# Performance work log

Hardware: AMD Instinct MI355X
Metric: run time of the kernel (lower is better)

The kernel has to match this reference:

```python
import jax, jax.numpy as jnp
import numpy as np

DIM = 768
HEADS = 12
HEAD_DIM = DIM // HEADS
HIDDEN = 4 * DIM
EPS = 1e-5
SCALE = HEAD_DIM ** -0.5


def _ln(x, g, b):
    mu = jnp.mean(x, axis=-1, keepdims=True)
    var = jnp.var(x, axis=-1, keepdims=True)
    return (x - mu) * jax.lax.rsqrt(var + EPS) * g + b


def setup_inputs() -> dict:
    key = jax.random.key(0)
    ks = jax.random.split(key, 10)
    s = lambda fan_in: 1.0 / np.sqrt(fan_in)
    return {
        "x": jax.random.normal(ks[0], (8, 4, 512, DIM), dtype=jnp.float32),
        "g1": jnp.ones((DIM,), jnp.float32),
        "b1": jnp.zeros((DIM,), jnp.float32),
        "Wqkv": jax.random.normal(ks[1], (DIM, 3 * DIM), jnp.float32) * s(DIM),
        "Wp": jax.random.normal(ks[2], (DIM, DIM), jnp.float32) * s(DIM),
        "bp": jnp.zeros((DIM,), jnp.float32),
        "g2": jnp.ones((DIM,), jnp.float32),
        "b2": jnp.zeros((DIM,), jnp.float32),
        "W1": jax.random.normal(ks[3], (DIM, HIDDEN), jnp.float32) * s(DIM),
        "bm1": jnp.zeros((HIDDEN,), jnp.float32),
        "W2": jax.random.normal(ks[4], (HIDDEN, DIM), jnp.float32) * s(HIDDEN),
        "bm2": jnp.zeros((DIM,), jnp.float32),
    }


def reference(x, g1, b1, Wqkv, Wp, bp, g2, b2, W1, bm1, W2, bm2):
    B, S, N, D = x.shape
    h = _ln(x, g1, b1)
    qkv = h @ Wqkv                                   # [B,S,N,3D]
    qkv = qkv.reshape(B, S, N, 3, HEADS, HEAD_DIM)
    q, k, v = (qkv[..., i, :, :] for i in range(3))  # [B,S,N,H,Dh]
    # scores over tokens N, per head
    attn = jnp.einsum("bsnhd,bsmhd->bshnm", q, k) * SCALE
    attn = jax.nn.softmax(attn, axis=-1)
    y = jnp.einsum("bshnm,bsmhd->bsnhd", attn, v).reshape(B, S, N, D)
    y = y @ Wp + bp
    x = x + y
    h2 = _ln(x, g2, b2)
    m = jax.nn.gelu(h2 @ W1 + bm1, approximate=False) @ W2 + bm2
    return x + m
```

## Files before the change

### kernel.cpp

```cpp
#include <hip/hip_runtime.h>
#include <hip/hip_bf16.h>
#include <cstdint>


typedef __bf16 bf16;
typedef bf16 bf16x8 __attribute__((ext_vector_type(8)));
typedef float f32x4 __attribute__((ext_vector_type(4)));
typedef uint32_t u32;

__device__ __forceinline__ f32x4 mfma16(bf16x8 a, bf16x8 b, f32x4 c){
  return __builtin_amdgcn_mfma_f32_16x16x32_bf16(a, b, c, 0, 0, 0);
}

__device__ __forceinline__ void gload16(const void* g, const void* l){
  __builtin_amdgcn_global_load_lds(
      (__attribute__((address_space(1))) u32*)(uintptr_t)g,
      (__attribute__((address_space(3))) u32*)(u32)(uintptr_t)l,
      16, 0, 0);
}

__global__ __launch_bounds__(256)
void transpose_cast(const float* __restrict__ W, bf16* __restrict__ Wt, int K, int N)
{
  __shared__ float t[64][65];
  int n0 = blockIdx.x * 64, k0 = blockIdx.y * 64;
  int tid = threadIdx.x;
  int c = tid & 63, r4 = tid >> 6;
#pragma unroll
  for (int i = 0; i < 16; ++i){
    int r = r4 * 16 + i;
    t[r][c] = W[(size_t)(k0 + r) * N + n0 + c];
  }
  __syncthreads();
#pragma unroll
  for (int i = 0; i < 16; ++i){
    int r = r4 * 16 + i;
    Wt[(size_t)(n0 + r) * K + k0 + c] = (bf16)t[c][r];
  }
}

__global__ __launch_bounds__(256)
void ln_kernel(const float* __restrict__ x, const float* __restrict__ g,
               const float* __restrict__ b, bf16* __restrict__ out)
{
  int row = blockIdx.x;
  int tid = threadIdx.x;
  const float* xr = x + (size_t)row * 768;
  float v0 = xr[tid], v1 = xr[tid + 256], v2 = xr[tid + 512];
  float s = v0 + v1 + v2;
  float ss = v0*v0 + v1*v1 + v2*v2;
#pragma unroll
  for (int m = 1; m < 64; m <<= 1){
    s  += __shfl_xor(s,  m, 64);
    ss += __shfl_xor(ss, m, 64);
  }
  __shared__ float red[8];
  int w = tid >> 6, l = tid & 63;
  if (l == 0){ red[w] = s; red[4 + w] = ss; }
  __syncthreads();
  s  = red[0] + red[1] + red[2] + red[3];
  ss = red[4] + red[5] + red[6] + red[7];
  float mu  = s * (1.0f / 768.0f);
  float var = ss * (1.0f / 768.0f) - mu * mu;
  float rs  = rsqrtf(var + 1e-5f);
  bf16* o = out + (size_t)row * 768;
  o[tid]       = (bf16)((v0 - mu) * rs * g[tid]       + b[tid]);
  o[tid + 256] = (bf16)((v1 - mu) * rs * g[tid + 256] + b[tid + 256]);
  o[tid + 512] = (bf16)((v2 - mu) * rs * g[tid + 512] + b[tid + 512]);
}

template<int EPI>
__global__ __launch_bounds__(256)
void gemm128(const bf16* __restrict__ A, const bf16* __restrict__ Bt,
             const float* __restrict__ bias, const float* __restrict__ res,
             void* __restrict__ Cout, int M, int N, int K)
{
  __shared__ bf16 Al[128 * 32];
  __shared__ bf16 Bl[128 * 32];
  int nbn = N >> 7;
  int nwg = gridDim.x;
  int cpx = nwg >> 3;
  int bid = (int)blockIdx.x;
  int sw  = (bid & 7) * cpx + (bid >> 3);
  int bm = sw / nbn, bn = sw % nbn;
  int tid = threadIdx.x;
  int w = tid >> 6, l = tid & 63;
  int wr = w >> 1, wc = w & 1;
  int lr = l & 15, lg = l >> 4;
  size_t rowA = (size_t)bm * 128, colB = (size_t)bn * 128;

  f32x4 acc[4][4];
#pragma unroll
  for (int m = 0; m < 4; ++m)
#pragma unroll
    for (int n = 0; n < 4; ++n) acc[m][n] = f32x4{0.f, 0.f, 0.f, 0.f};

  int rsub = l >> 2;
  int ksub = (l & 3) * 8;

  for (int kt = 0; kt < K; kt += 32){
    __syncthreads();
#pragma unroll
    for (int i = 0; i < 2; ++i){
      int sg = w * 2 + i;
      gload16(A  + (rowA + sg * 16 + rsub) * K + kt + ksub, &Al[sg * 512]);
      gload16(Bt + (colB + sg * 16 + rsub) * K + kt + ksub, &Bl[sg * 512]);
    }
    __syncthreads();
    bf16x8 af[4], bfr[4];
#pragma unroll
    for (int m = 0; m < 4; ++m)
      af[m]  = *(const bf16x8*)&Al[(wr * 64 + m * 16 + lr) * 32 + lg * 8];
#pragma unroll
    for (int n = 0; n < 4; ++n)
      bfr[n] = *(const bf16x8*)&Bl[(wc * 64 + n * 16 + lr) * 32 + lg * 8];
#pragma unroll
    for (int m = 0; m < 4; ++m)
#pragma unroll
      for (int n = 0; n < 4; ++n)
        acc[m][n] = mfma16(af[m], bfr[n], acc[m][n]);
  }

  size_t crow = rowA + wr * 64;
  size_t ccol = colB + wc * 64;
#pragma unroll
  for (int m = 0; m < 4; ++m){
#pragma unroll
    for (int n = 0; n < 4; ++n){
      size_t r0 = crow + m * 16 + lg * 4;
      size_t c  = ccol + n * 16 + lr;
#pragma unroll
      for (int i = 0; i < 4; ++i){
        size_t r = r0 + i;
        float v = acc[m][n][i];
        if (EPI == 0){
          ((bf16*)Cout)[r * (size_t)N + c] = (bf16)v;
        } else if (EPI == 1){
          v += bias[c];
          v = 0.5f * v * (1.0f + erff(v * 0.70710678118654752f));
          ((bf16*)Cout)[r * (size_t)N + c] = (bf16)v;
        } else {
          v += bias[c] + res[r * (size_t)N + c];
          ((float*)Cout)[r * (size_t)N + c] = v;
        }
      }
    }
  }
}

__global__ __launch_bounds__(256)
void attn_kernel(const bf16* __restrict__ qkv, bf16* __restrict__ y)
{
  int bid = blockIdx.x;
  int qt  = bid & 7;
  int bsh = bid >> 3;
  int h = bsh % 12;
  int R = bsh / 12;
  size_t rowbase = (size_t)R * 512;
  int tid = threadIdx.x, w = tid >> 6, l = tid & 63;
  int lr = l & 15, lg = l >> 4;

  __shared__ bf16 Kl[64 * 64];
  __shared__ bf16 Vt[64 * 64];
  __shared__ bf16 Pl[4][16 * 64];

  int q0 = qt * 64 + w * 16;
  bf16x8 qf[2];
#pragma unroll
  for (int ks = 0; ks < 2; ++ks)
    qf[ks] = *(const bf16x8*)&qkv[(rowbase + q0 + lr) * 2304 + h * 64 + ks * 32 + lg * 8];

  float mi[4], li[4];
  f32x4 oa[4];
#pragma unroll
  for (int i = 0; i < 4; ++i){ mi[i] = -1e30f; li[i] = 0.f; }
#pragma unroll
  for (int dt = 0; dt < 4; ++dt) oa[dt] = f32x4{0.f, 0.f, 0.f, 0.f};

  for (int c = 0; c < 8; ++c){
    __syncthreads();
    size_t tokbase = rowbase + c * 64;
#pragma unroll
    for (int it = 0; it < 2; ++it){
      int idx = it * 256 + tid;
      int t  = idx >> 3;
      int c8 = idx & 7;
      bf16x8 kv = *(const bf16x8*)&qkv[(tokbase + t) * 2304 + 768 + h * 64 + c8 * 8];
      *(bf16x8*)&Kl[t * 64 + ((c8 ^ (t & 7)) * 8)] = kv;
      bf16x8 vv = *(const bf16x8*)&qkv[(tokbase + t) * 2304 + 1536 + h * 64 + c8 * 8];
#pragma unroll
      for (int j = 0; j < 8; ++j){
        int d = c8 * 8 + j;
        Vt[d * 64 + (((t >> 3) ^ (d & 7)) * 8) + (t & 7)] = vv[j];
      }
    }
    __syncthreads();

    f32x4 s[4];
#pragma unroll
    for (int tt = 0; tt < 4; ++tt){
      f32x4 a = f32x4{0.f, 0.f, 0.f, 0.f};
#pragma unroll
      for (int ks = 0; ks < 2; ++ks){
        int row = tt * 16 + lr;
        int c8 = ks * 4 + lg;
        bf16x8 kf = *(const bf16x8*)&Kl[row * 64 + ((c8 ^ (row & 7)) * 8)];
        a = mfma16(qf[ks], kf, a);
      }
      s[tt] = a * 0.125f;
    }

    float pr[4][4];
#pragma unroll
    for (int i = 0; i < 4; ++i){
      float rm = fmaxf(fmaxf(s[0][i], s[1][i]), fmaxf(s[2][i], s[3][i]));
#pragma unroll
      for (int mm = 1; mm < 16; mm <<= 1) rm = fmaxf(rm, __shfl_xor(rm, mm, 64));
      float mn = fmaxf(mi[i], rm);
      float corr = __expf(mi[i] - mn);
      float rs = 0.f;
#pragma unroll
      for (int tt = 0; tt < 4; ++tt){
        float p = __expf(s[tt][i] - mn);
        pr[tt][i] = p;
        rs += p;
      }
#pragma unroll
      for (int mm = 1; mm < 16; mm <<= 1) rs += __shfl_xor(rs, mm, 64);
      li[i] = li[i] * corr + rs;
#pragma unroll
      for (int dt = 0; dt < 4; ++dt) oa[dt][i] *= corr;
      mi[i] = mn;
    }

#pragma unroll
    for (int i = 0; i < 4; ++i){
      int qr = lg * 4 + i;
#pragma unroll
      for (int tt = 0; tt < 4; ++tt){
        int tok = tt * 16 + lr;
        Pl[w][qr * 64 + (((tok >> 3) ^ (qr & 7)) * 8) + (tok & 7)] = (bf16)pr[tt][i];
      }
    }
    __syncthreads();

#pragma unroll
    for (int ks = 0; ks < 2; ++ks){
      bf16x8 pf = *(const bf16x8*)&Pl[w][lr * 64 + (((ks * 4 + lg) ^ (lr & 7)) * 8)];
#pragma unroll
      for (int dt = 0; dt < 4; ++dt){
        int row = dt * 16 + lr;
        int c8 = ks * 4 + lg;
        bf16x8 vf = *(const bf16x8*)&Vt[row * 64 + ((c8 ^ (row & 7)) * 8)];
        oa[dt] = mfma16(pf, vf, oa[dt]);
      }
    }
  }

#pragma unroll
  for (int i = 0; i < 4; ++i){
    float inv = 1.0f / li[i];
    size_t r = rowbase + q0 + lg * 4 + i;
#pragma unroll
    for (int dt = 0; dt < 4; ++dt)
      y[r * 768 + h * 64 + dt * 16 + lr] = (bf16)(oa[dt][i] * inv);
  }
}

extern "C" void kernel_launch(void* const* d_in, const int* in_sizes, int n_in,
                              void* d_out, int out_size, void* d_ws, size_t ws_size,
                              hipStream_t stream)
{
  (void)in_sizes; (void)n_in; (void)out_size; (void)ws_size;
  const float* x    = (const float*)d_in[0];
  const float* g1   = (const float*)d_in[1];
  const float* b1   = (const float*)d_in[2];
  const float* Wqkv = (const float*)d_in[3];
  const float* Wp   = (const float*)d_in[4];
  const float* bp   = (const float*)d_in[5];
  const float* g2   = (const float*)d_in[6];
  const float* b2   = (const float*)d_in[7];
  const float* W1   = (const float*)d_in[8];
  const float* bm1  = (const float*)d_in[9];
  const float* W2   = (const float*)d_in[10];
  const float* bm2  = (const float*)d_in[11];
  float* out = (float*)d_out;

  char* ws = (char*)d_ws;
  size_t off = 0;
  auto alloc = [&](size_t nbytes) -> void* {
    void* p = ws + off;
    off += (nbytes + 255) & ~(size_t)255;
    return p;
  };
  bf16* WqkvT = (bf16*)alloc((size_t)2304 * 768 * 2);
  bf16* WpT   = (bf16*)alloc((size_t)768 * 768 * 2);
  bf16* W1T   = (bf16*)alloc((size_t)3072 * 768 * 2);
  bf16* W2T   = (bf16*)alloc((size_t)768 * 3072 * 2);
  char* R1 = (char*)alloc((size_t)16384 * 768 * 2);
  char* R2 = (char*)alloc((size_t)16384 * 3072 * 2);
  bf16* h   = (bf16*)R1;
  bf16* yb  = (bf16*)R1;
  bf16* h2  = (bf16*)R1;
  bf16* qkv = (bf16*)R2;
  bf16* m1  = (bf16*)R2;
  float* x2 = out;

  transpose_cast<<<dim3(36, 12), dim3(256), 0, stream>>>(Wqkv, WqkvT, 768, 2304);
  transpose_cast<<<dim3(12, 12), dim3(256), 0, stream>>>(Wp,   WpT,   768, 768);
  transpose_cast<<<dim3(48, 12), dim3(256), 0, stream>>>(W1,   W1T,   768, 3072);
  transpose_cast<<<dim3(12, 48), dim3(256), 0, stream>>>(W2,   W2T,   3072, 768);

  ln_kernel<<<dim3(16384), dim3(256), 0, stream>>>(x, g1, b1, h);
  gemm128<0><<<dim3(2304), dim3(256), 0, stream>>>(h, WqkvT, nullptr, nullptr,
                                                   (void*)qkv, 16384, 2304, 768);
  attn_kernel<<<dim3(3072), dim3(256), 0, stream>>>(qkv, yb);
  gemm128<2><<<dim3(768), dim3(256), 0, stream>>>(yb, WpT, bp, x,
                                                  (void*)x2, 16384, 768, 768);
  ln_kernel<<<dim3(16384), dim3(256), 0, stream>>>(x2, g2, b2, h2);
  gemm128<1><<<dim3(3072), dim3(256), 0, stream>>>(h2, W1T, bm1, nullptr,
                                                   (void*)m1, 16384, 3072, 768);
  gemm128<2><<<dim3(768), dim3(256), 0, stream>>>(m1, W2T, bm2, x2,
                                                  (void*)out, 16384, 768, 3072);
}
```

Baseline: 700.6 us.

## Replace 128-tile GEMM with double-buffered 256x256 tile GEMM using swizzled LDS

```diff
diff --git a/kernel.cpp b/kernel.cpp
--- a/kernel.cpp
+++ b/kernel.cpp
@@ -70,69 +70,111 @@
 }
 
 template<int EPI>
-__global__ __launch_bounds__(256)
-void gemm128(const bf16* __restrict__ A, const bf16* __restrict__ Bt,
+__global__ __launch_bounds__(512, 2)
+void gemm256(const bf16* __restrict__ A, const bf16* __restrict__ Bt,
              const float* __restrict__ bias, const float* __restrict__ res,
              void* __restrict__ Cout, int M, int N, int K)
 {
-  __shared__ bf16 Al[128 * 32];
-  __shared__ bf16 Bl[128 * 32];
-  int nbn = N >> 7;
-  int nwg = gridDim.x;
-  int cpx = nwg >> 3;
-  int bid = (int)blockIdx.x;
-  int sw  = (bid & 7) * cpx + (bid >> 3);
-  int bm = sw / nbn, bn = sw % nbn;
-  int tid = threadIdx.x;
-  int w = tid >> 6, l = tid & 63;
-  int wr = w >> 1, wc = w & 1;
-  int lr = l & 15, lg = l >> 4;
-  size_t rowA = (size_t)bm * 128, colB = (size_t)bn * 128;
-
-  f32x4 acc[4][4];
-#pragma unroll
-  for (int m = 0; m < 4; ++m)
-#pragma unroll
-    for (int n = 0; n < 4; ++n) acc[m][n] = f32x4{0.f, 0.f, 0.f, 0.f};
-
-  int rsub = l >> 2;
-  int ksub = (l & 3) * 8;
-
-  for (int kt = 0; kt < K; kt += 32){
-    __syncthreads();
-#pragma unroll
-    for (int i = 0; i < 2; ++i){
-      int sg = w * 2 + i;
-      gload16(A  + (rowA + sg * 16 + rsub) * K + kt + ksub, &Al[sg * 512]);
-      gload16(Bt + (colB + sg * 16 + rsub) * K + kt + ksub, &Bl[sg * 512]);
-    }
-    __syncthreads();
-    bf16x8 af[4], bfr[4];
-#pragma unroll
-    for (int m = 0; m < 4; ++m)
-      af[m]  = *(const bf16x8*)&Al[(wr * 64 + m * 16 + lr) * 32 + lg * 8];
-#pragma unroll
-    for (int n = 0; n < 4; ++n)
-      bfr[n] = *(const bf16x8*)&Bl[(wc * 64 + n * 16 + lr) * 32 + lg * 8];
-#pragma unroll
-    for (int m = 0; m < 4; ++m)
-#pragma unroll
-      for (int n = 0; n < 4; ++n)
-        acc[m][n] = mfma16(af[m], bfr[n], acc[m][n]);
-  }
-
-  size_t crow = rowA + wr * 64;
-  size_t ccol = colB + wc * 64;
-#pragma unroll
-  for (int m = 0; m < 4; ++m){
-#pragma unroll
-    for (int n = 0; n < 4; ++n){
-      size_t r0 = crow + m * 16 + lg * 4;
-      size_t c  = ccol + n * 16 + lr;
+  extern __shared__ bf16 lds[];
+  const int tid = threadIdx.x;
+  const int w = tid >> 6, l = tid & 63;
+  const int lr = l & 15, lg = l >> 4;
+  const int wr = w >> 2, wc = w & 3;
+  const int nbm = M >> 8, nbn = N >> 8;
+  const int nwg = nbm * nbn;
+  const int cpx = nwg >> 3;
+  const int bid = (int)blockIdx.x;
+  const int sw  = (bid & 7) * cpx + (bid >> 3);
+  const int bm = sw % nbm, bn = sw / nbm;
+  const int rowA0 = bm << 8, colB0 = bn << 8;
+
+  f32x4 acc[8][4];
+#pragma unroll
+  for (int i = 0; i < 8; ++i)
+#pragma unroll
+    for (int j = 0; j < 4; ++j) acc[i][j] = f32x4{0.f, 0.f, 0.f, 0.f};
+
+  const int srow = l >> 3;
+  const int sg   = (l & 7) ^ srow;
+  auto stA = [&](int T, int q){
+    bf16* dst = lds + (size_t)(T & 1) * 32768 + q * 4096 + w * 512;
+    int row = q * 64 + w * 8 + srow;
+    gload16(A + (size_t)(rowA0 + row) * K + T * 64 + sg * 8, dst);
+  };
+  auto stB = [&](int T, int nh, int j){
+    int hh = j * 8 + w;
+    int row0 = (hh >> 2) * 64 + nh * 32 + (hh & 3) * 8;
+    bf16* dst = lds + (size_t)(T & 1) * 32768 + 16384 + row0 * 64;
+    int row = row0 + srow;
+    gload16(Bt + (size_t)(colB0 + row) * K + T * 64 + sg * 8, dst);
+  };
+
+  const int NT = K >> 6;
+
+  stA(0,0); stA(0,2); stB(0,0,0); stB(0,0,1);
+  stA(0,1); stA(0,3); stB(0,1,0); stB(0,1,1);
+  asm volatile("s_waitcnt vmcnt(4)" ::: "memory");
+  __builtin_amdgcn_s_barrier();
+
+#define PHASE(MH, NH, STAGE_STMT)                                              \
+  {                                                                            \
+    bf16x8 af[4][2], bfr[2][2];                                                \
+    _Pragma("unroll")                                                          \
+    for (int fr = 0; fr < 4; ++fr)                                             \
+      _Pragma("unroll")                                                        \
+      for (int kk = 0; kk < 2; ++kk){                                          \
+        int row = wr * 128 + (MH) * 64 + fr * 16 + lr;                         \
+        af[fr][kk] = *(const bf16x8*)&Abuf[row * 64 +                          \
+                       (((kk * 4 + lg) ^ (lr & 7)) << 3)];                     \
+      }                                                                        \
+    _Pragma("unroll")                                                          \
+    for (int fc = 0; fc < 2; ++fc)                                             \
+      _Pragma("unroll")                                                        \
+      for (int kk = 0; kk < 2; ++kk){                                          \
+        int row = wc * 64 + (NH) * 32 + fc * 16 + lr;                          \
+        bfr[fc][kk] = *(const bf16x8*)&Bbuf[row * 64 +                         \
+                       (((kk * 4 + lg) ^ (lr & 7)) << 3)];                     \
+      }                                                                        \
+    STAGE_STMT;                                                                \
+    if (more) asm volatile("s_waitcnt vmcnt(4)" ::: "memory");                 \
+    else      asm volatile("s_waitcnt vmcnt(0)" ::: "memory");                 \
+    __builtin_amdgcn_s_barrier();                                              \
+    __builtin_amdgcn_s_setprio(1);                                             \
+    _Pragma("unroll")                                                          \
+    for (int fr = 0; fr < 4; ++fr)                                             \
+      _Pragma("unroll")                                                        \
+      for (int fc = 0; fc < 2; ++fc)                                           \
+        _Pragma("unroll")                                                      \
+        for (int kk = 0; kk < 2; ++kk)                                         \
+          acc[(MH) * 4 + fr][(NH) * 2 + fc] =                                  \
+              mfma16(af[fr][kk], bfr[fc][kk], acc[(MH) * 4 + fr][(NH) * 2 + fc]); \
+    __builtin_amdgcn_s_setprio(0);                                             \
+    __builtin_amdgcn_s_barrier();                                              \
+  }
+
+  for (int T = 0; T < NT; ++T){
+    const bf16* Abuf = lds + (size_t)(T & 1) * 32768;
+    const bf16* Bbuf = Abuf + 16384;
+    const bool more = (T + 1 < NT);
+    PHASE(0, 0, if (more){ stA(T+1,0); stA(T+1,2); })
+    PHASE(1, 0, if (more){ stB(T+1,0,0); stB(T+1,0,1); })
+    PHASE(0, 1, if (more){ stA(T+1,1); stA(T+1,3); })
+    PHASE(1, 1, if (more){ stB(T+1,1,0); stB(T+1,1,1); })
+  }
+#undef PHASE
+
+  const size_t crow = (size_t)rowA0 + wr * 128;
+  const size_t ccol = (size_t)colB0 + wc * 64;
+#pragma unroll
+  for (int mi = 0; mi < 8; ++mi){
+#pragma unroll
+    for (int ni = 0; ni < 4; ++ni){
+      size_t r0 = crow + (mi >> 2) * 64 + (mi & 3) * 16 + lg * 4;
+      size_t c  = ccol + (ni >> 1) * 32 + (ni & 1) * 16 + lr;
 #pragma unroll
       for (int i = 0; i < 4; ++i){
         size_t r = r0 + i;
-        float v = acc[m][n][i];
+        float v = acc[mi][ni][i];
         if (EPI == 0){
           ((bf16*)Cout)[r * (size_t)N + c] = (bf16)v;
         } else if (EPI == 1){
@@ -285,6 +327,10 @@
   const float* W2   = (const float*)d_in[10];
   const float* bm2  = (const float*)d_in[11];
   float* out = (float*)d_out;
+
+  hipFuncSetAttribute((const void*)gemm256<0>, hipFuncAttributeMaxDynamicSharedMemorySize, 131072);
+  hipFuncSetAttribute((const void*)gemm256<1>, hipFuncAttributeMaxDynamicSharedMemorySize, 131072);
+  hipFuncSetAttribute((const void*)gemm256<2>, hipFuncAttributeMaxDynamicSharedMemorySize, 131072);
 
   char* ws = (char*)d_ws;
   size_t off = 0;
@@ -312,14 +358,14 @@
   transpose_cast<<<dim3(12, 48), dim3(256), 0, stream>>>(W2,   W2T,   3072, 768);
 
   ln_kernel<<<dim3(16384), dim3(256), 0, stream>>>(x, g1, b1, h);
-  gemm128<0><<<dim3(2304), dim3(256), 0, stream>>>(h, WqkvT, nullptr, nullptr,
-                                                   (void*)qkv, 16384, 2304, 768);
+  gemm256<0><<<dim3(576), dim3(512), 131072, stream>>>(h, WqkvT, nullptr, nullptr,
+                                                       (void*)qkv, 16384, 2304, 768);
   attn_kernel<<<dim3(3072), dim3(256), 0, stream>>>(qkv, yb);
-  gemm128<2><<<dim3(768), dim3(256), 0, stream>>>(yb, WpT, bp, x,
-                                                  (void*)x2, 16384, 768, 768);
+  gemm256<2><<<dim3(192), dim3(512), 131072, stream>>>(yb, WpT, bp, x,
+                                                       (void*)x2, 16384, 768, 768);
   ln_kernel<<<dim3(16384), dim3(256), 0, stream>>>(x2, g2, b2, h2);
-  gemm128<1><<<dim3(3072), dim3(256), 0, stream>>>(h2, W1T, bm1, nullptr,
-                                                   (void*)m1, 16384, 3072, 768);
-  gemm128<2><<<dim3(768), dim3(256), 0, stream>>>(m1, W2T, bm2, x2,
-                                                  (void*)out, 16384, 768, 3072);
-}
+  gemm256<1><<<dim3(768), dim3(512), 131072, stream>>>(h2, W1T, bm1, nullptr,
+                                                       (void*)m1, 16384, 3072, 768);
+  gemm256<2><<<dim3(192), dim3(512), 131072, stream>>>(m1, W2T, bm2, x2,
+                                                       (void*)out, 16384, 768, 3072);
+}
```

Result: faster. 658.6 us (-6.0%).
